# Kernel tuning notes

Measured on AMD Instinct MI355X. Metric: run time of the kernel, lower is better.

Reference implementation:

```python
import jax, jax.numpy as jnp
import numpy as np

N = 40000        # total gene nodes
E = 640000       # edges
F_IN = 128       # num_features
H = 128          # hidden_dim
SUB = 400        # genes per cell
EPS = 1e-5


def _bn(x, g, b):
    # BatchNorm1d, training-mode batch statistics (biased variance), deterministic
    m = x.mean(axis=0)
    v = x.var(axis=0)
    return (x - m) * jax.lax.rsqrt(v + EPS) * g + b


def _gcn_conv(x, W, b, src, dst):
    # PyG GCNConv: h = X W; add self-loops; symmetric deg^{-1/2} normalization;
    # scatter-add messages from src into dst; then add bias.
    h = x @ W                                   # [N, H]
    loop = jnp.arange(N)
    s = jnp.concatenate([src, loop])            # [E+N]
    d = jnp.concatenate([dst, loop])
    deg = jax.ops.segment_sum(jnp.ones(s.shape[0], h.dtype), d, num_segments=N)
    dis = jnp.where(deg > 0, deg ** -0.5, 0.0)  # deg_inv_sqrt
    norm = dis[s] * dis[d]                      # [E+N]
    out = jax.ops.segment_sum(h[s] * norm[:, None], d, num_segments=N)
    return out + b


def setup_inputs() -> dict:
    key = jax.random.key(0)
    ks = jax.random.split(key, 16)
    sc = lambda fan: 1.0 / np.sqrt(fan)
    inp = {
        "x": jax.random.normal(ks[0], (N, F_IN), jnp.float32),
        "edge_index": jax.random.randint(ks[1], (2, E), 0, N, jnp.int64),
        "conv1_w": jax.random.normal(ks[2], (F_IN, H), jnp.float32) * sc(F_IN),
        "conv1_b": jnp.zeros((H,), jnp.float32),
        "bn1_g": jnp.ones((H,), jnp.float32),
        "bn1_b": jnp.zeros((H,), jnp.float32),
        "conv2_w": jax.random.normal(ks[3], (H, H), jnp.float32) * sc(H),
        "conv2_b": jnp.zeros((H,), jnp.float32),
        "bn2_g": jnp.ones((H,), jnp.float32),
        "bn2_b": jnp.zeros((H,), jnp.float32),
        "att_w1": jax.random.normal(ks[4], (H, H // 2), jnp.float32) * sc(H),
        "att_b1": jnp.zeros((H // 2,), jnp.float32),
        "att_w2": jax.random.normal(ks[5], (H // 2, 1), jnp.float32) * sc(H // 2),
        "att_b2": jnp.zeros((1,), jnp.float32),
        "fc_w": jax.random.normal(ks[6], (H, H), jnp.float32) * sc(H),
        "fc_b": jnp.zeros((H,), jnp.float32),
        "bne_g": jnp.ones((H,), jnp.float32),
        "bne_b": jnp.zeros((H,), jnp.float32),
        "bot_w": jax.random.normal(ks[7], (H, 32), jnp.float32) * sc(H),
        "bot_b": jnp.zeros((32,), jnp.float32),
        "bnb_g": jnp.ones((32,), jnp.float32),
        "bnb_b": jnp.zeros((32,), jnp.float32),
    }
    return inp


def reference(x, edge_index, conv1_w, conv1_b, bn1_g, bn1_b,
              conv2_w, conv2_b, bn2_g, bn2_b,
              att_w1, att_b1, att_w2, att_b2,
              fc_w, fc_b, bne_g, bne_b,
              bot_w, bot_b, bnb_g, bnb_b):
    src, dst = edge_index[0], edge_index[1]
    # embed: two GCNConv + BN + ReLU (dropout omitted: deterministic reference)
    h = jax.nn.relu(_bn(_gcn_conv(x, conv1_w, conv1_b, src, dst), bn1_g, bn1_b))
    emb = jax.nn.relu(_bn(_gcn_conv(h, conv2_w, conv2_b, src, dst), bn2_g, bn2_b))
    # attention pooling over genes within each cell
    num_cells = N // SUB
    xr = emb.reshape(num_cells, SUB, H)                      # [C, S, H]
    scores = jnp.tanh(xr @ att_w1 + att_b1) @ att_w2 + att_b2  # [C, S, 1]
    w = jax.nn.softmax(scores, axis=1)
    pooled = jnp.sum(xr * w, axis=1)                          # [C, H]
    # dense head
    y = jax.nn.relu(_bn(pooled @ fc_w + fc_b, bne_g, bne_b))
    y = jax.nn.relu(_bn(y @ bot_w + bot_b, bnb_g, bnb_b))     # [C, 32]
    return (y, emb)
```

## Files before the change

kernel.cpp:

```cpp
#include <hip/hip_runtime.h>
#include <math.h>

typedef unsigned int u32;
typedef unsigned short u16;
typedef __attribute__((ext_vector_type(8))) short bf16x8;
typedef __attribute__((ext_vector_type(4))) float f32x4;

#define NN   40000
#define EE   640000
#define SUBG 400
#define CELLS 100
#define BNEPS 1e-5f
#define GB    2048
#define GEMMB 625
#define DEGB  1024
#define FILLB 1024

__device__ __forceinline__ u32 bf16pair(float a, float b) {
    u32 ua = __float_as_uint(a), ub = __float_as_uint(b);
    ua += 0x7fffu + ((ua >> 16) & 1u);
    ub += 0x7fffu + ((ub >> 16) & 1u);
    return (ua >> 16) | (ub & 0xffff0000u);
}
__device__ __forceinline__ float bflo(u32 u) { return __uint_as_float(u << 16); }
__device__ __forceinline__ float bfhi(u32 u) { return __uint_as_float(u & 0xffff0000u); }

__global__ void k_init(int* deg_cursor, const float* W1, u32* Wt1,
                       const float* W2, u32* Wt2, const float* wa, u32* Wta,
                       float* hstats) {
    int i = blockIdx.x * 256 + threadIdx.x;
    if (i < 2 * NN) { deg_cursor[i] = 0; return; }
    i -= 2 * NN;
    if (i < 16384) {
        const float* W = (i < 8192) ? W1 : W2;
        u32* Wt = (i < 8192) ? Wt1 : Wt2;
        int j = i & 8191;
        int n = j >> 6, k2 = (j & 63) * 2;
        Wt[n * 64 + (j & 63)] = bf16pair(W[k2 * 128 + n], W[(k2 + 1) * 128 + n]);
        return;
    }
    i -= 16384;
    if (i < 4096) {
        int n = i >> 6, k2 = (i & 63) * 2;
        Wta[n * 64 + (i & 63)] = bf16pair(wa[k2 * 64 + n], wa[(k2 + 1) * 64 + n]);
        return;
    }
    i -= 4096;
    if (i < 320) hstats[i] = 0.f;
}

__global__ void k_degcount(const int* __restrict__ dst, int* __restrict__ deg) {
    int i = blockIdx.x * blockDim.x + threadIdx.x;
    int stride = DEGB * 256;
    for (; i < EE; i += stride) atomicAdd(&deg[dst[i]], 1);
}

__global__ __launch_bounds__(1024)
void k_scan(const int* __restrict__ deg, int* __restrict__ rowstart,
            float* __restrict__ dis) {
    __shared__ int ps[1024];
    int t = threadIdx.x;
    const int4* d4 = (const int4*)deg;
    int sum = 0;
#pragma unroll
    for (int j = 0; j < 10; ++j) {
        int i4 = t * 10 + j;
        if (i4 < 10000) {
            int4 v = d4[i4];
            sum += v.x + v.y + v.z + v.w;
        }
    }
    ps[t] = sum;
    __syncthreads();
    for (int off = 1; off < 1024; off <<= 1) {
        int add = (t >= off) ? ps[t - off] : 0;
        __syncthreads();
        ps[t] += add;
        __syncthreads();
    }
    int run = ps[t] - sum;
#pragma unroll
    for (int j = 0; j < 10; ++j) {
        int i4 = t * 10 + j;
        if (i4 < 10000) {
            int4 v = d4[i4];
            int4 r;
            r.x = run;
            r.y = run + v.x;
            r.z = r.y + v.y;
            r.w = r.z + v.z;
            run = r.w + v.w;
            *(int4*)&rowstart[i4 * 4] = r;
            float4 dv;
            dv.x = rsqrtf((float)(v.x + 1));
            dv.y = rsqrtf((float)(v.y + 1));
            dv.z = rsqrtf((float)(v.z + 1));
            dv.w = rsqrtf((float)(v.w + 1));
            *(float4*)&dis[i4 * 4] = dv;
        }
    }
    if (t == 0) rowstart[NN] = EE;
}

__global__ __launch_bounds__(256)
void k_fillgemm(const int* __restrict__ src, const int* __restrict__ dst,
                const int* __restrict__ rowstart, int* __restrict__ cursor,
                u16* __restrict__ csr16,
                const float* __restrict__ X, const u32* __restrict__ Wt,
                u32* __restrict__ Yb, const float* __restrict__ dis) {
    int bid = blockIdx.x;
    int t = threadIdx.x;
    if (bid < FILLB) {
        int i = bid * 256 + t;
        int stride = FILLB * 256;
        for (; i < EE; i += stride) {
            int d = dst[i];
            int slot = rowstart[d] + atomicAdd(&cursor[d], 1);
            csr16[slot] = (u16)src[i];
        }
        return;
    }
    int l = t & 63, wv = t >> 6;
    int rowbase = (bid - FILLB) * 64 + wv * 16;
    int ml = l & 15, kg = l >> 4;

    f32x4 acc[8];
#pragma unroll
    for (int nt = 0; nt < 8; ++nt) acc[nt] = (f32x4){0.f, 0.f, 0.f, 0.f};
    const float* xr = X + (long)(rowbase + ml) * 128;
#pragma unroll
    for (int kk = 0; kk < 4; ++kk) {
        int k0 = kk * 32 + kg * 8;
        float4 xa = *(const float4*)&xr[k0];
        float4 xb = *(const float4*)&xr[k0 + 4];
        union { u32 u[4]; bf16x8 v; } af;
        af.u[0] = bf16pair(xa.x, xa.y);
        af.u[1] = bf16pair(xa.z, xa.w);
        af.u[2] = bf16pair(xb.x, xb.y);
        af.u[3] = bf16pair(xb.z, xb.w);
#pragma unroll
        for (int nt = 0; nt < 8; ++nt) {
            bf16x8 b = *(const bf16x8*)&Wt[(nt * 16 + ml) * 64 + (k0 >> 1)];
            acc[nt] = __builtin_amdgcn_mfma_f32_16x16x32_bf16(af.v, b, acc[nt], 0, 0, 0);
        }
    }
#pragma unroll
    for (int r = 0; r < 4; ++r) {
        int m = rowbase + kg * 4 + r;
        float dd = dis[m];
        long obase = (long)m * 64;
#pragma unroll
        for (int nt = 0; nt < 8; ++nt) {
            float v = acc[nt][r] * dd;
            float v2 = __shfl_xor(v, 1);
            if ((l & 1) == 0)
                Yb[obase + nt * 8 + (ml >> 1)] = bf16pair(v, v2);
        }
    }
}

__global__ __launch_bounds__(256)
void k_gemm_bf16(const u32* __restrict__ Xb, const u32* __restrict__ Wt,
                 u32* __restrict__ Yb, const float* __restrict__ ss,
                 const float* __restrict__ dis) {
    int t = threadIdx.x;
    int l = t & 63, wv = t >> 6;
    int rowbase = blockIdx.x * 64 + wv * 16;
    int ml = l & 15, kg = l >> 4;

    f32x4 acc[8];
#pragma unroll
    for (int nt = 0; nt < 8; ++nt) acc[nt] = (f32x4){0.f, 0.f, 0.f, 0.f};
    const u32* xr = Xb + (long)(rowbase + ml) * 64;
#pragma unroll
    for (int kk = 0; kk < 4; ++kk) {
        int k0 = kk * 32 + kg * 8;
        uint4 xw = *(const uint4*)&xr[k0 >> 1];
        float f0 = bflo(xw.x), f1 = bfhi(xw.x), f2 = bflo(xw.y), f3 = bfhi(xw.y);
        float f4 = bflo(xw.z), f5 = bfhi(xw.z), f6 = bflo(xw.w), f7 = bfhi(xw.w);
        float4 sca = *(const float4*)&ss[k0];
        float4 sha = *(const float4*)&ss[128 + k0];
        float4 scb = *(const float4*)&ss[k0 + 4];
        float4 shb = *(const float4*)&ss[128 + k0 + 4];
        f0 = fmaxf(fmaf(f0, sca.x, sha.x), 0.f);
        f1 = fmaxf(fmaf(f1, sca.y, sha.y), 0.f);
        f2 = fmaxf(fmaf(f2, sca.z, sha.z), 0.f);
        f3 = fmaxf(fmaf(f3, sca.w, sha.w), 0.f);
        f4 = fmaxf(fmaf(f4, scb.x, shb.x), 0.f);
        f5 = fmaxf(fmaf(f5, scb.y, shb.y), 0.f);
        f6 = fmaxf(fmaf(f6, scb.z, shb.z), 0.f);
        f7 = fmaxf(fmaf(f7, scb.w, shb.w), 0.f);
        union { u32 u[4]; bf16x8 v; } af;
        af.u[0] = bf16pair(f0, f1);
        af.u[1] = bf16pair(f2, f3);
        af.u[2] = bf16pair(f4, f5);
        af.u[3] = bf16pair(f6, f7);
#pragma unroll
        for (int nt = 0; nt < 8; ++nt) {
            bf16x8 b = *(const bf16x8*)&Wt[(nt * 16 + ml) * 64 + (k0 >> 1)];
            acc[nt] = __builtin_amdgcn_mfma_f32_16x16x32_bf16(af.v, b, acc[nt], 0, 0, 0);
        }
    }
#pragma unroll
    for (int r = 0; r < 4; ++r) {
        int m = rowbase + kg * 4 + r;
        float dd = dis[m];
        long obase = (long)m * 64;
#pragma unroll
        for (int nt = 0; nt < 8; ++nt) {
            float v = acc[nt][r] * dd;
            float v2 = __shfl_xor(v, 1);
            if ((l & 1) == 0)
                Yb[obase + nt * 8 + (ml >> 1)] = bf16pair(v, v2);
        }
    }
}

__global__ __launch_bounds__(256)
void k_gather_stats(const uint4* __restrict__ Hb, const int* __restrict__ rowstart,
                    const u16* __restrict__ csr16, const float* __restrict__ dis,
                    const float* __restrict__ bias, u32* __restrict__ F1b,
                    float* __restrict__ part) {
    __shared__ float ls[1024], lq[1024];
    int t = threadIdx.x;
    int lane = t & 63, wv = t >> 6;
    int gw = blockIdx.x * 4 + wv;
    int g = lane >> 4, p = lane & 15;
    int c0 = p * 8 + g * 2;
    float2 bb = *(const float2*)&bias[c0];
    float s0 = 0.f, s1 = 0.f, q0 = 0.f, q1 = 0.f;

    for (int node = gw; node < NN; node += GB * 4) {
        float a0 = 0.f, a1 = 0.f, a2 = 0.f, a3 = 0.f, a4 = 0.f, a5 = 0.f, a6 = 0.f, a7 = 0.f;
        if (g == 0) {
            uint4 h = Hb[node * 16 + p];
            a0 = bflo(h.x); a1 = bfhi(h.x);
            a2 = bflo(h.y); a3 = bfhi(h.y);
            a4 = bflo(h.z); a5 = bfhi(h.z);
            a6 = bflo(h.w); a7 = bfhi(h.w);
        }
        int e1 = rowstart[node + 1];
        int e = rowstart[node] + g;
        for (; e + 4 < e1; e += 8) {
            int sA = csr16[e];
            int sB = csr16[e + 4];
            uint4 h0 = Hb[sA * 16 + p];
            uint4 h1 = Hb[sB * 16 + p];
            a0 += bflo(h0.x); a1 += bfhi(h0.x);
            a2 += bflo(h0.y); a3 += bfhi(h0.y);
            a4 += bflo(h0.z); a5 += bfhi(h0.z);
            a6 += bflo(h0.w); a7 += bfhi(h0.w);
            a0 += bflo(h1.x); a1 += bfhi(h1.x);
            a2 += bflo(h1.y); a3 += bfhi(h1.y);
            a4 += bflo(h1.z); a5 += bfhi(h1.z);
            a6 += bflo(h1.w); a7 += bfhi(h1.w);
        }
        if (e < e1) {
            int sA = csr16[e];
            uint4 h0 = Hb[sA * 16 + p];
            a0 += bflo(h0.x); a1 += bfhi(h0.x);
            a2 += bflo(h0.y); a3 += bfhi(h0.y);
            a4 += bflo(h0.z); a5 += bfhi(h0.z);
            a6 += bflo(h0.w); a7 += bfhi(h0.w);
        }
#pragma unroll
        for (int m = 16; m <= 32; m <<= 1) {
            a0 += __shfl_xor(a0, m); a1 += __shfl_xor(a1, m);
            a2 += __shfl_xor(a2, m); a3 += __shfl_xor(a3, m);
            a4 += __shfl_xor(a4, m); a5 += __shfl_xor(a5, m);
            a6 += __shfl_xor(a6, m); a7 += __shfl_xor(a7, m);
        }
        float dd = dis[node];
        float x = (g == 0) ? a0 : (g == 1) ? a2 : (g == 2) ? a4 : a6;
        float y = (g == 0) ? a1 : (g == 1) ? a3 : (g == 2) ? a5 : a7;
        x = fmaf(x, dd, bb.x);
        y = fmaf(y, dd, bb.y);
        u32 pw = bf16pair(x, y);
        F1b[node * 64 + (c0 >> 1)] = pw;
        float rx = bflo(pw), ry = bfhi(pw);
        s0 += rx; s1 += ry; q0 += rx * rx; q1 += ry * ry;
    }
    ls[wv * 128 + c0] = s0; ls[wv * 128 + c0 + 1] = s1;
    lq[wv * 128 + c0] = q0; lq[wv * 128 + c0 + 1] = q1;
    __syncthreads();
    if (t < 128) {
        float S = ls[t] + ls[128 + t] + ls[256 + t] + ls[384 + t];
        float Q = lq[t] + lq[128 + t] + lq[256 + t] + lq[384 + t];
        part[blockIdx.x * 256 + t] = S;
        part[blockIdx.x * 256 + 128 + t] = Q;
    }
}

__global__ __launch_bounds__(256)
void k_bnfinalw(const float* __restrict__ part, const float* __restrict__ g,
                const float* __restrict__ b, float* __restrict__ ss) {
    __shared__ float rs[256], rq[256];
    int c = blockIdx.x, t = threadIdx.x;
    float s = 0.f, q = 0.f;
    for (int i = t; i < GB; i += 256) {
        s += part[i * 256 + c];
        q += part[i * 256 + 128 + c];
    }
    rs[t] = s; rq[t] = q;
    __syncthreads();
    for (int off = 128; off > 0; off >>= 1) {
        if (t < off) { rs[t] += rs[t + off]; rq[t] += rq[t + off]; }
        __syncthreads();
    }
    if (t == 0) {
        float mean = rs[0] * (1.0f / NN);
        float var  = rq[0] * (1.0f / NN) - mean * mean;
        float sc = g[c] * rsqrtf(var + BNEPS);
        ss[c] = sc;
        ss[128 + c] = b[c] - mean * sc;
    }
}

__global__ __launch_bounds__(256)
void k_scoremb(const u32* __restrict__ F1b, const float* __restrict__ ss,
               float* __restrict__ emb,
               const u32* __restrict__ Wta, const float* __restrict__ b1,
               const float* __restrict__ w2, const float* __restrict__ b2,
               float* __restrict__ scores) {
    int t = threadIdx.x;
    int l = t & 63, wv = t >> 6;
    int rowbase = blockIdx.x * 64 + wv * 16;
    int ml = l & 15, kg = l >> 4;

    f32x4 acc[4];
#pragma unroll
    for (int nt = 0; nt < 4; ++nt) acc[nt] = (f32x4){0.f, 0.f, 0.f, 0.f};
    const u32* xr = F1b + (long)(rowbase + ml) * 64;
    float* er = emb + (long)(rowbase + ml) * 128;
#pragma unroll
    for (int kk = 0; kk < 4; ++kk) {
        int k0 = kk * 32 + kg * 8;
        uint4 xw = *(const uint4*)&xr[k0 >> 1];
        float f0 = bflo(xw.x), f1 = bfhi(xw.x), f2 = bflo(xw.y), f3 = bfhi(xw.y);
        float f4 = bflo(xw.z), f5 = bfhi(xw.z), f6 = bflo(xw.w), f7 = bfhi(xw.w);
        float4 sca = *(const float4*)&ss[k0];
        float4 sha = *(const float4*)&ss[128 + k0];
        float4 scb = *(const float4*)&ss[k0 + 4];
        float4 shb = *(const float4*)&ss[128 + k0 + 4];
        f0 = fmaxf(fmaf(f0, sca.x, sha.x), 0.f);
        f1 = fmaxf(fmaf(f1, sca.y, sha.y), 0.f);
        f2 = fmaxf(fmaf(f2, sca.z, sha.z), 0.f);
        f3 = fmaxf(fmaf(f3, sca.w, sha.w), 0.f);
        f4 = fmaxf(fmaf(f4, scb.x, shb.x), 0.f);
        f5 = fmaxf(fmaf(f5, scb.y, shb.y), 0.f);
        f6 = fmaxf(fmaf(f6, scb.z, shb.z), 0.f);
        f7 = fmaxf(fmaf(f7, scb.w, shb.w), 0.f);
        float4 e0 = { f0, f1, f2, f3 };
        float4 e1 = { f4, f5, f6, f7 };
        *(float4*)&er[k0] = e0;
        *(float4*)&er[k0 + 4] = e1;
        union { u32 u[4]; bf16x8 v; } af;
        af.u[0] = bf16pair(f0, f1);
        af.u[1] = bf16pair(f2, f3);
        af.u[2] = bf16pair(f4, f5);
        af.u[3] = bf16pair(f6, f7);
#pragma unroll
        for (int nt = 0; nt < 4; ++nt) {
            bf16x8 b = *(const bf16x8*)&Wta[(nt * 16 + ml) * 64 + (k0 >> 1)];
            acc[nt] = __builtin_amdgcn_mfma_f32_16x16x32_bf16(af.v, b, acc[nt], 0, 0, 0);
        }
    }
    float b1v[4], w2v[4];
#pragma unroll
    for (int nt = 0; nt < 4; ++nt) {
        b1v[nt] = b1[nt * 16 + ml];
        w2v[nt] = w2[nt * 16 + ml];
    }
    float b2v = b2[0];
#pragma unroll
    for (int r = 0; r < 4; ++r) {
        float s = tanhf(acc[0][r] + b1v[0]) * w2v[0]
                + tanhf(acc[1][r] + b1v[1]) * w2v[1]
                + tanhf(acc[2][r] + b1v[2]) * w2v[2]
                + tanhf(acc[3][r] + b1v[3]) * w2v[3];
        s += __shfl_xor(s, 1);
        s += __shfl_xor(s, 2);
        s += __shfl_xor(s, 4);
        s += __shfl_xor(s, 8);
        if (ml == 0) scores[rowbase + kg * 4 + r] = s + b2v;
    }
}

__global__ __launch_bounds__(256)
void k_pool4(const u32* __restrict__ F1b, const float* __restrict__ ss,
             const float* __restrict__ scores, float* __restrict__ pp) {
    __shared__ float sl[SUBG];
    __shared__ float red[256];
    __shared__ float rbuf[512];
    int b = blockIdx.x;
    int c = b >> 2, q = b & 3;
    int t = threadIdx.x;
    int base = c * SUBG;

    float lmax = -1e30f;
    for (int i = t; i < SUBG; i += 256) {
        float v = scores[base + i];
        sl[i] = v;
        lmax = fmaxf(lmax, v);
    }
    red[t] = lmax;
    __syncthreads();
    for (int off = 128; off > 0; off >>= 1) {
        if (t < off) red[t] = fmaxf(red[t], red[t + off]);
        __syncthreads();
    }
    float mx = red[0];
    __syncthreads();
    float lsum = 0.f;
    for (int i = t; i < SUBG; i += 256) {
        float e = __expf(sl[i] - mx);
        sl[i] = e;
        lsum += e;
    }
    red[t] = lsum;
    __syncthreads();
    for (int off = 128; off > 0; off >>= 1) {
        if (t < off) red[t] += red[t + off];
        __syncthreads();
    }
    float inv = 1.0f / red[0];
    __syncthreads();

    int cc = t & 63, gp = t >> 6;
    float2 scv = *(const float2*)&ss[2 * cc];
    float2 shv = *(const float2*)&ss[128 + 2 * cc];
    int g0 = q * 100 + gp * 25;
    float a0 = 0.f, a1 = 0.f;
#pragma unroll 5
    for (int j = 0; j < 25; ++j) {
        int gg = g0 + j;
        u32 v = F1b[(long)(base + gg) * 64 + cc];
        float w = sl[gg] * inv;
        float x0 = fmaxf(fmaf(bflo(v), scv.x, shv.x), 0.f);
        float x1 = fmaxf(fmaf(bfhi(v), scv.y, shv.y), 0.f);
        a0 += w * x0;
        a1 += w * x1;
    }
    rbuf[gp * 128 + 2 * cc] = a0;
    rbuf[gp * 128 + 2 * cc + 1] = a1;
    __syncthreads();
    if (t < 128)
        pp[b * 128 + t] = rbuf[t] + rbuf[128 + t] + rbuf[256 + t] + rbuf[384 + t];
}

__global__ __launch_bounds__(128)
void k_head1r(const float* __restrict__ pp, const float* __restrict__ fc_w,
              const float* __restrict__ fc_b, float* __restrict__ y1pre,
              float* __restrict__ hstats) {
    __shared__ float pr[128];
    int c = blockIdx.x, t = threadIdx.x;
    pr[t] = pp[(c * 4 + 0) * 128 + t] + pp[(c * 4 + 1) * 128 + t]
          + pp[(c * 4 + 2) * 128 + t] + pp[(c * 4 + 3) * 128 + t];
    __syncthreads();
    float a1 = fc_b[t];
#pragma unroll 4
    for (int k = 0; k < 128; ++k) a1 = fmaf(pr[k], fc_w[k * 128 + t], a1);
    y1pre[c * 128 + t] = a1;
    atomicAdd(&hstats[t], a1);
    atomicAdd(&hstats[128 + t], a1 * a1);
}

__global__ __launch_bounds__(128)
void k_head2s(const float* __restrict__ y1pre, const float* __restrict__ hstats,
              const float* __restrict__ bne_g, const float* __restrict__ bne_b,
              const float* __restrict__ bot_w, const float* __restrict__ bot_b,
              float* __restrict__ y2pre, float* __restrict__ hstats2) {
    __shared__ float row[128];
    int c = blockIdx.x, t = threadIdx.x;
    float s = hstats[t], q = hstats[128 + t];
    float mean = s * 0.01f, var = q * 0.01f - mean * mean;
    float scv = bne_g[t] * rsqrtf(var + BNEPS);
    float shv = bne_b[t] - mean * scv;
    row[t] = fmaxf(fmaf(y1pre[c * 128 + t], scv, shv), 0.f);
    __syncthreads();
    if (t < 32) {
        float a2 = bot_b[t];
#pragma unroll 4
        for (int k = 0; k < 128; ++k) a2 = fmaf(row[k], bot_w[k * 32 + t], a2);
        y2pre[c * 32 + t] = a2;
        atomicAdd(&hstats2[t], a2);
        atomicAdd(&hstats2[32 + t], a2 * a2);
    }
}

__global__ __launch_bounds__(256)
void k_out(const float* __restrict__ y2pre, const float* __restrict__ hstats2,
           const float* __restrict__ bnb_g, const float* __restrict__ bnb_b,
           float* __restrict__ y_out) {
    __shared__ float scv[32], shv[32];
    int t = threadIdx.x;
    if (t < 32) {
        float s = hstats2[t], q = hstats2[32 + t];
        float mean = s * 0.01f, var = q * 0.01f - mean * mean;
        float v = bnb_g[t] * rsqrtf(var + BNEPS);
        scv[t] = v; shv[t] = bnb_b[t] - mean * v;
    }
    __syncthreads();
    for (int i = t; i < CELLS * 32; i += 256)
        y_out[i] = fmaxf(fmaf(y2pre[i], scv[i & 31], shv[i & 31]), 0.f);
}

extern "C" void kernel_launch(void* const* d_in, const int* in_sizes, int n_in,
                              void* d_out, int out_size, void* d_ws, size_t ws_size,
                              hipStream_t stream) {
    const float* x        = (const float*)d_in[0];
    const int*   ei       = (const int*)d_in[1];
    const float* conv1_w  = (const float*)d_in[2];
    const float* conv1_b  = (const float*)d_in[3];
    const float* bn1_g    = (const float*)d_in[4];
    const float* bn1_b    = (const float*)d_in[5];
    const float* conv2_w  = (const float*)d_in[6];
    const float* conv2_b  = (const float*)d_in[7];
    const float* bn2_g    = (const float*)d_in[8];
    const float* bn2_b    = (const float*)d_in[9];
    const float* att_w1   = (const float*)d_in[10];
    const float* att_b1   = (const float*)d_in[11];
    const float* att_w2   = (const float*)d_in[12];
    const float* att_b2   = (const float*)d_in[13];
    const float* fc_w     = (const float*)d_in[14];
    const float* fc_b     = (const float*)d_in[15];
    const float* bne_g    = (const float*)d_in[16];
    const float* bne_b    = (const float*)d_in[17];
    const float* bot_w    = (const float*)d_in[18];
    const float* bot_b    = (const float*)d_in[19];
    const float* bnb_g    = (const float*)d_in[20];
    const float* bnb_b    = (const float*)d_in[21];

    const int* src = ei;
    const int* dst = ei + EE;

    float* y_out   = (float*)d_out;
    float* emb_out = y_out + CELLS * 32;

    float* ws = (float*)d_ws;
    u32*   Hb     = (u32*)ws;
    u32*   F1b    = Hb + (long)NN * 64;
    float* dis    = (float*)(F1b + (long)NN * 64);
    float* part   = dis + NN;
    float* ss     = part + GB * 256;
    float* hstats = ss + 256;
    float* y1pre  = hstats + 320;
    float* y2pre  = y1pre + CELLS * 128;
    float* scores = y2pre + CELLS * 32;
    float* pp     = scores + NN;
    u32*   Wt1    = (u32*)(pp + 400 * 128);
    u32*   Wt2    = Wt1 + 8192;
    u32*   Wta    = Wt2 + 8192;
    int*   deg    = (int*)(Wta + 4096);
    int*   cursor = deg + NN;
    int*   rowstart = cursor + NN;
    u16*   csr16  = (u16*)(rowstart + NN + 1);

    k_init<<<394, 256, 0, stream>>>(deg, conv1_w, Wt1, conv2_w, Wt2, att_w1, Wta, hstats);
    k_degcount<<<DEGB, 256, 0, stream>>>(dst, deg);
    k_scan<<<1, 1024, 0, stream>>>(deg, rowstart, dis);
    k_fillgemm<<<FILLB + GEMMB, 256, 0, stream>>>(src, dst, rowstart, cursor, csr16,
                                                  x, Wt1, Hb, dis);
    k_gather_stats<<<GB, 256, 0, stream>>>((const uint4*)Hb, rowstart, csr16, dis,
                                           conv1_b, F1b, part);
    k_bnfinalw<<<128, 256, 0, stream>>>(part, bn1_g, bn1_b, ss);
    k_gemm_bf16<<<GEMMB, 256, 0, stream>>>(F1b, Wt2, Hb, ss, dis);
    k_gather_stats<<<GB, 256, 0, stream>>>((const uint4*)Hb, rowstart, csr16, dis,
                                           conv2_b, F1b, part);
    k_bnfinalw<<<128, 256, 0, stream>>>(part, bn2_g, bn2_b, ss);
    k_scoremb<<<GEMMB, 256, 0, stream>>>(F1b, ss, emb_out, Wta, att_b1, att_w2,
                                         att_b2, scores);
    k_pool4<<<4 * CELLS, 256, 0, stream>>>(F1b, ss, scores, pp);
    k_head1r<<<CELLS, 128, 0, stream>>>(pp, fc_w, fc_b, y1pre, hstats);
    k_head2s<<<CELLS, 128, 0, stream>>>(y1pre, hstats, bne_g, bne_b, bot_w, bot_b,
                                        y2pre, hstats + 256);
    k_out<<<1, 256, 0, stream>>>(y2pre, hstats + 256, bnb_g, bnb_b, y_out);
}
```

Before: 240.1 us.

## Fuse degree count with weight conversion and partition CSR fill by destination range

Degree counting and bf16 weight transposition now share one kernel, and the counter zeroing moves to a memset. Zeroing of the head statistics moves into the scan kernel. The CSR fill blocks are split into 8 groups, each owning one eighth of the destination nodes, so atomics and scattered writes from a group stay in a narrower address range for better cache locality. The cost is that every group reads the whole dst array, so edge reads grow eightfold, and there are half as many fill blocks.

```diff
diff --git a/kernel.cpp b/kernel.cpp
--- a/kernel.cpp
+++ b/kernel.cpp
@@ -14,7 +14,7 @@
 #define GB    2048
 #define GEMMB 625
 #define DEGB  1024
-#define FILLB 1024
+#define FILLB 512
 
 __device__ __forceinline__ u32 bf16pair(float a, float b) {
     u32 ua = __float_as_uint(a), ub = __float_as_uint(b);
@@ -25,12 +25,20 @@
 __device__ __forceinline__ float bflo(u32 u) { return __uint_as_float(u << 16); }
 __device__ __forceinline__ float bfhi(u32 u) { return __uint_as_float(u & 0xffff0000u); }
 
-__global__ void k_init(int* deg_cursor, const float* W1, u32* Wt1,
-                       const float* W2, u32* Wt2, const float* wa, u32* Wta,
-                       float* hstats) {
-    int i = blockIdx.x * 256 + threadIdx.x;
-    if (i < 2 * NN) { deg_cursor[i] = 0; return; }
-    i -= 2 * NN;
+__global__ __launch_bounds__(256)
+void k_degW(const int* __restrict__ dst, int* __restrict__ deg,
+            const float* __restrict__ W1, u32* __restrict__ Wt1,
+            const float* __restrict__ W2, u32* __restrict__ Wt2,
+            const float* __restrict__ wa, u32* __restrict__ Wta) {
+    int bid = blockIdx.x;
+    int t = threadIdx.x;
+    if (bid < DEGB) {
+        int i = bid * 256 + t;
+        int stride = DEGB * 256;
+        for (; i < EE; i += stride) atomicAdd(&deg[dst[i]], 1);
+        return;
+    }
+    int i = (bid - DEGB) * 256 + t;
     if (i < 16384) {
         const float* W = (i < 8192) ? W1 : W2;
         u32* Wt = (i < 8192) ? Wt1 : Wt2;
@@ -43,23 +51,15 @@
     if (i < 4096) {
         int n = i >> 6, k2 = (i & 63) * 2;
         Wta[n * 64 + (i & 63)] = bf16pair(wa[k2 * 64 + n], wa[(k2 + 1) * 64 + n]);
-        return;
-    }
-    i -= 4096;
-    if (i < 320) hstats[i] = 0.f;
-}
-
-__global__ void k_degcount(const int* __restrict__ dst, int* __restrict__ deg) {
-    int i = blockIdx.x * blockDim.x + threadIdx.x;
-    int stride = DEGB * 256;
-    for (; i < EE; i += stride) atomicAdd(&deg[dst[i]], 1);
+    }
 }
 
 __global__ __launch_bounds__(1024)
 void k_scan(const int* __restrict__ deg, int* __restrict__ rowstart,
-            float* __restrict__ dis) {
+            float* __restrict__ dis, float* __restrict__ hstats) {
     __shared__ int ps[1024];
     int t = threadIdx.x;
+    if (t < 320) hstats[t] = 0.f;
     const int4* d4 = (const int4*)deg;
     int sum = 0;
 #pragma unroll
@@ -111,12 +111,16 @@
     int bid = blockIdx.x;
     int t = threadIdx.x;
     if (bid < FILLB) {
-        int i = bid * 256 + t;
-        int stride = FILLB * 256;
+        int g = bid & 7;
+        int lo = g * (NN / 8), hi = lo + (NN / 8);
+        int i = (bid >> 3) * 256 + t;
+        int stride = (FILLB / 8) * 256;
         for (; i < EE; i += stride) {
             int d = dst[i];
-            int slot = rowstart[d] + atomicAdd(&cursor[d], 1);
-            csr16[slot] = (u16)src[i];
+            if (d >= lo && d < hi) {
+                int slot = rowstart[d] + atomicAdd(&cursor[d], 1);
+                csr16[slot] = (u16)src[i];
+            }
         }
         return;
     }
@@ -556,9 +560,10 @@
     int*   rowstart = cursor + NN;
     u16*   csr16  = (u16*)(rowstart + NN + 1);
 
-    k_init<<<394, 256, 0, stream>>>(deg, conv1_w, Wt1, conv2_w, Wt2, att_w1, Wta, hstats);
-    k_degcount<<<DEGB, 256, 0, stream>>>(dst, deg);
-    k_scan<<<1, 1024, 0, stream>>>(deg, rowstart, dis);
+    hipMemsetAsync(deg, 0, (size_t)2 * NN * sizeof(int), stream);
+    k_degW<<<DEGB + 80, 256, 0, stream>>>(dst, deg, conv1_w, Wt1, conv2_w, Wt2,
+                                          att_w1, Wta);
+    k_scan<<<1, 1024, 0, stream>>>(deg, rowstart, dis, hstats);
     k_fillgemm<<<FILLB + GEMMB, 256, 0, stream>>>(src, dst, rowstart, cursor, csr16,
                                                   x, Wt1, Hb, dis);
     k_gather_stats<<<GB, 256, 0, stream>>>((const uint4*)Hb, rowstart, csr16, dis,
```

New measurement: 242.7 us. About the same (+1.1%).
